# Kernel tuning notes

Measured on AMD Instinct MI355X. Metric: run time of the kernel, lower is better.

## Reference

```python
import jax, jax.numpy as jnp
import numpy as np

N_NODES = 100000
N_EDGES = 600000
N_GRAPHS = 4096
F_IN = 74
H = 128
L = 3
BN_EPS = 1e-5


def setup_inputs() -> dict:
    key = jax.random.key(0)
    ks = jax.random.split(key, 12)
    x = jax.random.normal(ks[0], (N_NODES, F_IN), dtype=jnp.float32)
    edge_index = jax.random.randint(ks[1], (2, N_EDGES), 0, N_NODES)
    batch = jnp.sort(jax.random.randint(ks[2], (N_NODES,), 0, N_GRAPHS))

    def lin(k, fan_in, fan_out):
        return (jax.random.normal(k, (fan_in, fan_out), dtype=jnp.float32)
                / np.float32(np.sqrt(fan_in)))

    emb_W = lin(ks[3], F_IN, H)
    emb_b = jnp.zeros((H,), jnp.float32)
    conv_W = jax.random.normal(ks[4], (L, H, H), dtype=jnp.float32) / np.float32(np.sqrt(H))
    conv_b = jnp.zeros((L, H), jnp.float32)
    bn_gamma = jnp.ones((L, H), jnp.float32)
    bn_beta = jnp.zeros((L, H), jnp.float32)
    w1 = lin(ks[5], 2 * H, H)
    b1 = jnp.zeros((H,), jnp.float32)
    w2 = lin(ks[6], H, H // 2)
    b2 = jnp.zeros((H // 2,), jnp.float32)
    w3 = lin(ks[7], H // 2, 1)
    b3 = jnp.zeros((1,), jnp.float32)
    return dict(x=x, edge_index=edge_index, batch=batch,
                emb_W=emb_W, emb_b=emb_b, conv_W=conv_W, conv_b=conv_b,
                bn_gamma=bn_gamma, bn_beta=bn_beta,
                w1=w1, b1=b1, w2=w2, b2=b2, w3=w3, b3=b3)


def reference(x, edge_index, batch, emb_W, emb_b, conv_W, conv_b,
              bn_gamma, bn_beta, w1, b1, w2, b2, w3, b3):
    N = x.shape[0]
    # GCN normalization with self-loops (PyG GCNConv semantics)
    loops = jnp.arange(N)
    src = jnp.concatenate([edge_index[0], loops])  # [E+N]
    dst = jnp.concatenate([edge_index[1], loops])
    deg = jax.ops.segment_sum(jnp.ones_like(dst, jnp.float32), dst, num_segments=N)
    dinv = jax.lax.rsqrt(jnp.maximum(deg, 1.0))  # deg >= 1 due to self-loops
    norm = dinv[src] * dinv[dst]                 # [E+N]

    h = jax.nn.relu(x @ emb_W + emb_b)           # [N, H]
    for i in range(L):
        hw = h @ conv_W[i]                       # [N, H]
        msg = hw[src] * norm[:, None]            # gather + scale  [E+N, H]
        h = jax.ops.segment_sum(msg, dst, num_segments=N) + conv_b[i]
        # BatchNorm1d, training-mode batch statistics (biased variance)
        mu = jnp.mean(h, axis=0)
        var = jnp.mean((h - mu) ** 2, axis=0)
        h = (h - mu) * jax.lax.rsqrt(var + BN_EPS) * bn_gamma[i] + bn_beta[i]
        h = jax.nn.relu(h)
        # dropout: identity (inference / deterministic baseline)

    # segment mean / max pooling over graphs
    cnt = jax.ops.segment_sum(jnp.ones((N,), jnp.float32), batch, num_segments=N_GRAPHS)
    g_mean = jax.ops.segment_sum(h, batch, num_segments=N_GRAPHS) / jnp.maximum(cnt, 1.0)[:, None]
    g_max = jax.ops.segment_max(h, batch, num_segments=N_GRAPHS)
    g_max = jnp.where(jnp.isfinite(g_max), g_max, 0.0)  # guard empty segments
    g = jnp.concatenate([g_mean, g_max], axis=1)         # [G, 2H]

    h1 = jax.nn.relu(g @ w1 + b1)
    h2 = jax.nn.relu(h1 @ w2 + b2)
    return h2 @ w3 + b3                                   # [G, 1]
```

## Files before the change

kernel.cpp:

```cpp
#include <hip/hip_runtime.h>

#define NN 100000
#define NE 600000
#define NG 4096
#define FIN 74
#define HD 128
#define NL 3
#define BN_EPS 1e-5f
#define NSCAN 391

typedef __attribute__((ext_vector_type(8))) short short8;
typedef __attribute__((ext_vector_type(4))) float floatx4;
typedef __attribute__((ext_vector_type(8))) unsigned short bf16x8;
typedef __attribute__((ext_vector_type(4))) unsigned short bf16x4;

__device__ __forceinline__ unsigned short f2bf(float f) {
    unsigned u = __float_as_uint(f);
    u += 0x7fff + ((u >> 16) & 1);
    return (unsigned short)(u >> 16);
}
__device__ __forceinline__ float bf2f(unsigned short u) {
    return __uint_as_float(((unsigned)u) << 16);
}

__global__ __launch_bounds__(256) void k_hist(const int* __restrict__ dst,
                                              int* __restrict__ degi) {
    int e = blockIdx.x * 256 + threadIdx.x;
    if (e < NE) atomicAdd(&degi[dst[e]], 1);
}

__global__ __launch_bounds__(256) void k_scan1(const int* __restrict__ degi,
                                               int* __restrict__ part) {
    __shared__ int s[256];
    int t = threadIdx.x;
    int idx = blockIdx.x * 256 + t;
    s[t] = (idx < NN) ? degi[idx] : 0;
    __syncthreads();
    for (int off = 128; off > 0; off >>= 1) {
        if (t < off) s[t] += s[t + off];
        __syncthreads();
    }
    if (t == 0) part[blockIdx.x] = s[0];
}

__global__ __launch_bounds__(512) void k_scan2(int* __restrict__ part) {
    __shared__ int s[512];
    int t = threadIdx.x;
    s[t] = (t < NSCAN) ? part[t] : 0;
    __syncthreads();
    for (int off = 1; off < 512; off <<= 1) {
        int v = s[t];
        int a = (t >= off) ? s[t - off] : 0;
        __syncthreads();
        s[t] = v + a;
        __syncthreads();
    }
    if (t < NSCAN) part[t] = (t > 0) ? s[t - 1] : 0;
}

__global__ __launch_bounds__(256) void k_scan3(const int* __restrict__ degi,
                                               const int* __restrict__ part,
                                               int* __restrict__ rowptr,
                                               float* __restrict__ dinv) {
    __shared__ int s[256];
    int t = threadIdx.x;
    int idx = blockIdx.x * 256 + t;
    int v = (idx < NN) ? degi[idx] : 0;
    s[t] = v;
    __syncthreads();
    for (int off = 1; off < 256; off <<= 1) {
        int x = s[t];
        int a = (t >= off) ? s[t - off] : 0;
        __syncthreads();
        s[t] = x + a;
        __syncthreads();
    }
    if (idx < NN) {
        rowptr[idx] = part[blockIdx.x] + (s[t] - v);
        dinv[idx] = rsqrtf((float)v + 1.0f);
    }
    if (idx == 0) rowptr[NN] = NE;
}

__global__ __launch_bounds__(256) void k_fill(const int* __restrict__ src,
                                              const int* __restrict__ dst,
                                              const int* __restrict__ rowptr,
                                              int* __restrict__ cursor,
                                              int* __restrict__ col) {
    int e = blockIdx.x * 256 + threadIdx.x;
    if (e >= NE) return;
    int d = dst[e];
    int pos = rowptr[d] + atomicAdd(&cursor[d], 1);
    col[pos] = src[e];
}

__global__ __launch_bounds__(256) void k_bounds(const int* __restrict__ batch,
                                                int* __restrict__ gstart) {
    int n = blockIdx.x * 256 + threadIdx.x;
    if (n >= NN) return;
    int b = batch[n];
    int bp = (n == 0) ? -1 : batch[n - 1];
    for (int g = bp + 1; g <= b; g++) gstart[g] = n;
    if (n == NN - 1)
        for (int g = b + 1; g <= NG; g++) gstart[g] = NN;
}

__global__ __launch_bounds__(256) void k_wpack(const float* __restrict__ embW,
                                               const float* __restrict__ convW,
                                               unsigned short* __restrict__ WfE,
                                               unsigned short* __restrict__ WfC) {
    int d = blockIdx.x * 256 + threadIdx.x;
    if (d < 12288) {
        int inner = d & 511, outer = d >> 9;
        int kstep = outer % 3, nt = outer / 3;
        int g = inner >> 7, n = (inner >> 3) & 15, j = inner & 7;
        int k = kstep * 32 + g * 8 + j;
        float v = (k < FIN) ? embW[k * HD + nt * 16 + n] : 0.0f;
        WfE[d] = f2bf(v);
    } else {
        int e = d - 12288;
        if (e >= NL * 16384) return;
        int layer = e >> 14, r = e & 16383;
        int j = r & 7, n = (r >> 3) & 15, g = (r >> 7) & 3, kstep = (r >> 9) & 3, nt = r >> 11;
        int k = kstep * 32 + g * 8 + j;
        WfC[e] = f2bf(convW[layer * 16384 + k * HD + nt * 16 + n]);
    }
}

__global__ __launch_bounds__(256) void k_emb(const float* __restrict__ x,
                                             const unsigned short* __restrict__ Wf,
                                             const float* __restrict__ b,
                                             unsigned short* __restrict__ hA) {
    __shared__ __align__(16) unsigned short As[4224];
    int t = threadIdx.x;
    int n0 = blockIdx.x * 32;
    for (int f = t; f < 3072; f += 256) {
        int m = f / 96, kp = f % 96;
        float v = (kp < FIN) ? x[(n0 + m) * FIN + kp] : 0.0f;
        int kstep = kp >> 5, g = (kp >> 3) & 3, j = kp & 7;
        As[(kstep * 4 + g) * 264 + m * 8 + j] = f2bf(v);
    }
    __syncthreads();
    int lane = t & 63, wv = t >> 6;
    int lanelo = lane & 15, g = lane >> 4;
    floatx4 acc[2][2] = {};
#pragma unroll
    for (int kstep = 0; kstep < 3; kstep++) {
        short8 a0 = *(const short8*)&As[(kstep * 4 + g) * 264 + lanelo * 8];
        short8 a1 = *(const short8*)&As[(kstep * 4 + g) * 264 + 128 + lanelo * 8];
        short8 b0 = *(const short8*)&Wf[(((wv * 2 + 0) * 3 + kstep) * 4 + g) * 128 + lanelo * 8];
        short8 b1 = *(const short8*)&Wf[(((wv * 2 + 1) * 3 + kstep) * 4 + g) * 128 + lanelo * 8];
        acc[0][0] = __builtin_amdgcn_mfma_f32_16x16x32_bf16(a0, b0, acc[0][0], 0, 0, 0);
        acc[0][1] = __builtin_amdgcn_mfma_f32_16x16x32_bf16(a0, b1, acc[0][1], 0, 0, 0);
        acc[1][0] = __builtin_amdgcn_mfma_f32_16x16x32_bf16(a1, b0, acc[1][0], 0, 0, 0);
        acc[1][1] = __builtin_amdgcn_mfma_f32_16x16x32_bf16(a1, b1, acc[1][1], 0, 0, 0);
    }
    __syncthreads();
#pragma unroll
    for (int ns = 0; ns < 2; ns++) {
        int colc = wv * 32 + ns * 16 + lanelo;
        float bias = b[colc];
#pragma unroll
        for (int ms = 0; ms < 2; ms++)
#pragma unroll
            for (int r = 0; r < 4; r++) {
                int rowl = ms * 16 + g * 4 + r;
                As[rowl * 132 + colc] = f2bf(fmaxf(acc[ms][ns][r] + bias, 0.0f));
            }
    }
    __syncthreads();
#pragma unroll
    for (int i = 0; i < 2; i++) {
        int f = t * 8 + i * 2048;
        int m = f >> 7, c = f & 127;
        bf16x4 lo = *(const bf16x4*)&As[m * 132 + c];
        bf16x4 hi = *(const bf16x4*)&As[m * 132 + c + 4];
        bf16x8 o = {lo.x, lo.y, lo.z, lo.w, hi.x, hi.y, hi.z, hi.w};
        *(bf16x8*)&hA[n0 * HD + f] = o;
    }
}

template <bool BN>
__global__ __launch_bounds__(256) void k_conv(const unsigned short* __restrict__ hin,
                                              const float* __restrict__ ss,
                                              const unsigned short* __restrict__ Wf,
                                              const float* __restrict__ dinv,
                                              unsigned short* __restrict__ hw) {
    __shared__ __align__(16) unsigned short As[4224];
    __shared__ float dinvs[32];
    int t = threadIdx.x;
    int n0 = blockIdx.x * 32;
    if (t < 32) dinvs[t] = dinv[n0 + t];
    int f0 = t * 8;
    int k0 = f0 & 127;
    float sc[8], sh[8];
    if (BN) {
        floatx4 s0 = *(const floatx4*)&ss[k0];
        floatx4 s1 = *(const floatx4*)&ss[k0 + 4];
        floatx4 h0 = *(const floatx4*)&ss[HD + k0];
        floatx4 h1 = *(const floatx4*)&ss[HD + k0 + 4];
        sc[0] = s0.x; sc[1] = s0.y; sc[2] = s0.z; sc[3] = s0.w;
        sc[4] = s1.x; sc[5] = s1.y; sc[6] = s1.z; sc[7] = s1.w;
        sh[0] = h0.x; sh[1] = h0.y; sh[2] = h0.z; sh[3] = h0.w;
        sh[4] = h1.x; sh[5] = h1.y; sh[6] = h1.z; sh[7] = h1.w;
    }
    int combo = (k0 >> 5) * 4 + ((k0 >> 3) & 3);
#pragma unroll
    for (int i = 0; i < 2; i++) {
        int f = f0 + i * 2048;
        int m = f >> 7;
        bf16x8 u = *(const bf16x8*)&hin[n0 * HD + f];
        bf16x8 o;
        if (BN) {
#pragma unroll
            for (int jj = 0; jj < 8; jj++) {
                float v = fmaxf(bf2f(u[jj]) * sc[jj] + sh[jj], 0.0f);
                o[jj] = f2bf(v);
            }
        } else {
            o = u;
        }
        *(bf16x8*)&As[combo * 264 + m * 8] = o;
    }
    __syncthreads();
    int lane = t & 63, wv = t >> 6;
    int lanelo = lane & 15, g = lane >> 4;
    floatx4 acc[2][2] = {};
#pragma unroll
    for (int ks = 0; ks < 4; ks++) {
        short8 a0 = *(const short8*)&As[(ks * 4 + g) * 264 + lanelo * 8];
        short8 a1 = *(const short8*)&As[(ks * 4 + g) * 264 + 128 + lanelo * 8];
        short8 b0 = *(const short8*)&Wf[(((wv * 2 + 0) * 4 + ks) * 4 + g) * 128 + lanelo * 8];
        short8 b1 = *(const short8*)&Wf[(((wv * 2 + 1) * 4 + ks) * 4 + g) * 128 + lanelo * 8];
        acc[0][0] = __builtin_amdgcn_mfma_f32_16x16x32_bf16(a0, b0, acc[0][0], 0, 0, 0);
        acc[0][1] = __builtin_amdgcn_mfma_f32_16x16x32_bf16(a0, b1, acc[0][1], 0, 0, 0);
        acc[1][0] = __builtin_amdgcn_mfma_f32_16x16x32_bf16(a1, b0, acc[1][0], 0, 0, 0);
        acc[1][1] = __builtin_amdgcn_mfma_f32_16x16x32_bf16(a1, b1, acc[1][1], 0, 0, 0);
    }
    __syncthreads();
#pragma unroll
    for (int ms = 0; ms < 2; ms++)
#pragma unroll
        for (int ns = 0; ns < 2; ns++) {
            int colc = wv * 32 + ns * 16 + lanelo;
#pragma unroll
            for (int r = 0; r < 4; r++) {
                int rowl = ms * 16 + g * 4 + r;
                As[rowl * 132 + colc] = f2bf(acc[ms][ns][r] * dinvs[rowl]);
            }
        }
    __syncthreads();
#pragma unroll
    for (int i = 0; i < 2; i++) {
        int f = f0 + i * 2048;
        int m = f >> 7, c = f & 127;
        bf16x4 lo = *(const bf16x4*)&As[m * 132 + c];
        bf16x4 hi = *(const bf16x4*)&As[m * 132 + c + 4];
        bf16x8 o = {lo.x, lo.y, lo.z, lo.w, hi.x, hi.y, hi.z, hi.w};
        *(bf16x8*)&hw[n0 * HD + f] = o;
    }
}

__global__ __launch_bounds__(256) void k_gather(const int* __restrict__ rowptr,
                                                const int* __restrict__ col,
                                                const float* __restrict__ dinv,
                                                const unsigned short* __restrict__ B,
                                                const float* __restrict__ bias,
                                                unsigned short* __restrict__ A) {
    int t = threadIdx.x;
    int n = blockIdx.x * 16 + (t >> 4);
    int c8 = (t & 15) * 8;
    bf16x8 u = *(const bf16x8*)&B[n * HD + c8];
    float acc[8];
#pragma unroll
    for (int i = 0; i < 8; i++) acc[i] = bf2f(u[i]);
    int j0 = rowptr[n], j1 = rowptr[n + 1];
    int j = j0;
    for (; j + 1 < j1; j += 2) {
        int s0 = col[j], s1 = col[j + 1];
        bf16x8 v0 = *(const bf16x8*)&B[s0 * HD + c8];
        bf16x8 v1 = *(const bf16x8*)&B[s1 * HD + c8];
#pragma unroll
        for (int i = 0; i < 8; i++) acc[i] += bf2f(v0[i]) + bf2f(v1[i]);
    }
    if (j < j1) {
        int s = col[j];
        bf16x8 v = *(const bf16x8*)&B[s * HD + c8];
#pragma unroll
        for (int i = 0; i < 8; i++) acc[i] += bf2f(v[i]);
    }
    float dd = dinv[n];
    floatx4 b0 = *(const floatx4*)&bias[c8];
    floatx4 b1 = *(const floatx4*)&bias[c8 + 4];
    bf16x8 o;
    o[0] = f2bf(acc[0] * dd + b0.x); o[1] = f2bf(acc[1] * dd + b0.y);
    o[2] = f2bf(acc[2] * dd + b0.z); o[3] = f2bf(acc[3] * dd + b0.w);
    o[4] = f2bf(acc[4] * dd + b1.x); o[5] = f2bf(acc[5] * dd + b1.y);
    o[6] = f2bf(acc[6] * dd + b1.z); o[7] = f2bf(acc[7] * dd + b1.w);
    *(bf16x8*)&A[n * HD + c8] = o;
}

__global__ __launch_bounds__(256) void k_bn_stats(const unsigned short* __restrict__ h,
                                                  float* __restrict__ sums) {
    __shared__ float ls[256];
    int t = threadIdx.x;
    ls[t] = 0.0f;
    __syncthreads();
    int c8 = (t & 15) * 8;
    float s[8] = {}, sq[8] = {};
    for (int n = blockIdx.x * 16 + (t >> 4); n < NN; n += gridDim.x * 16) {
        bf16x8 u = *(const bf16x8*)&h[n * HD + c8];
#pragma unroll
        for (int i = 0; i < 8; i++) {
            float v = bf2f(u[i]);
            s[i] += v;
            sq[i] += v * v;
        }
    }
#pragma unroll
    for (int i = 0; i < 8; i++) {
        atomicAdd(&ls[c8 + i], s[i]);
        atomicAdd(&ls[HD + c8 + i], sq[i]);
    }
    __syncthreads();
    atomicAdd(&sums[t], ls[t]);
}

__global__ __launch_bounds__(128) void k_bn_fin(const float* __restrict__ sums,
                                                const float* __restrict__ gamma,
                                                const float* __restrict__ beta,
                                                float* __restrict__ ss) {
    int c = threadIdx.x;
    float inv_n = 1.0f / (float)NN;
    float mu = sums[c] * inv_n;
    float var = sums[HD + c] * inv_n - mu * mu;
    float sc = gamma[c] * rsqrtf(var + BN_EPS);
    ss[c] = sc;
    ss[HD + c] = beta[c] - mu * sc;
}

__global__ __launch_bounds__(128) void k_pool_g(const unsigned short* __restrict__ h,
                                                const float* __restrict__ ss,
                                                const int* __restrict__ gstart,
                                                float* __restrict__ gfeat) {
    int g = blockIdx.x;
    int c = threadIdx.x;
    int n0 = gstart[g], n1 = gstart[g + 1];
    float sc = ss[c], sh = ss[HD + c];
    float s = 0.0f, mx = 0.0f;
    for (int n = n0; n < n1; n++) {
        float v = fmaxf(bf2f(h[n * HD + c]) * sc + sh, 0.0f);
        s += v;
        mx = fmaxf(mx, v);
    }
    float cntf = (float)(n1 - n0);
    gfeat[g * 256 + c] = s / fmaxf(cntf, 1.0f);
    gfeat[g * 256 + HD + c] = mx;
}

__global__ __launch_bounds__(256) void k_mlp(const float* __restrict__ gfeat,
                                             const float* __restrict__ w1,
                                             const float* __restrict__ b1,
                                             const float* __restrict__ w2,
                                             const float* __restrict__ b2,
                                             const float* __restrict__ w3,
                                             const float* __restrict__ b3,
                                             float* __restrict__ out) {
    __shared__ float gs[8][258];
    __shared__ float p1[8][130];
    __shared__ float hs[8][130];
    __shared__ float p2[3][8][66];
    __shared__ float h2s[8][66];
    __shared__ float ps[64];
    int t = threadIdx.x;
    int g0 = blockIdx.x * 8;
    for (int f = t; f < 2048; f += 256) {
        int gi = f >> 8, k = f & 255;
        gs[gi][k] = gfeat[(g0 + gi) * 256 + k];
    }
    __syncthreads();
    {
        int colc = t & 127, half = t >> 7;
        int kb = half * 128;
        float acc[8] = {};
        for (int k = 0; k < 128; k++) {
            float w = w1[(kb + k) * HD + colc];
#pragma unroll
            for (int gi = 0; gi < 8; gi++) acc[gi] += gs[gi][kb + k] * w;
        }
        if (half == 1) {
#pragma unroll
            for (int gi = 0; gi < 8; gi++) p1[gi][colc] = acc[gi];
        }
        __syncthreads();
        if (half == 0) {
            float bias = b1[colc];
#pragma unroll
            for (int gi = 0; gi < 8; gi++)
                hs[gi][colc] = fmaxf(acc[gi] + p1[gi][colc] + bias, 0.0f);
        }
    }
    __syncthreads();
    {
        int colc = t & 63, q = t >> 6;
        int kb = q * 32;
        float acc[8] = {};
        for (int k = 0; k < 32; k++) {
            float w = w2[(kb + k) * 64 + colc];
#pragma unroll
            for (int gi = 0; gi < 8; gi++) acc[gi] += hs[gi][kb + k] * w;
        }
        if (q > 0) {
#pragma unroll
            for (int gi = 0; gi < 8; gi++) p2[q - 1][gi][colc] = acc[gi];
        }
        __syncthreads();
        if (q == 0) {
            float bias = b2[colc];
#pragma unroll
            for (int gi = 0; gi < 8; gi++)
                h2s[gi][colc] = fmaxf(acc[gi] + p2[0][gi][colc] + p2[1][gi][colc]
                                      + p2[2][gi][colc] + bias, 0.0f);
        }
    }
    __syncthreads();
    if (t < 64) {
        int gi = t >> 3, prt = t & 7;
        float p = 0.0f;
#pragma unroll
        for (int k = 0; k < 8; k++) p += h2s[gi][prt * 8 + k] * w3[prt * 8 + k];
        ps[t] = p;
    }
    __syncthreads();
    if (t < 8) {
        float a = b3[0];
#pragma unroll
        for (int i = 0; i < 8; i++) a += ps[t * 8 + i];
        out[g0 + t] = a;
    }
}

extern "C" void kernel_launch(void* const* d_in, const int* in_sizes, int n_in,
                              void* d_out, int out_size, void* d_ws, size_t ws_size,
                              hipStream_t stream) {
    const float* x      = (const float*)d_in[0];
    const int*   eidx   = (const int*)d_in[1];
    const int*   batch  = (const int*)d_in[2];
    const float* emb_W  = (const float*)d_in[3];
    const float* emb_b  = (const float*)d_in[4];
    const float* conv_W = (const float*)d_in[5];
    const float* conv_b = (const float*)d_in[6];
    const float* gamma  = (const float*)d_in[7];
    const float* beta   = (const float*)d_in[8];
    const float* w1     = (const float*)d_in[9];
    const float* b1     = (const float*)d_in[10];
    const float* w2     = (const float*)d_in[11];
    const float* b2     = (const float*)d_in[12];
    const float* w3     = (const float*)d_in[13];
    const float* b3     = (const float*)d_in[14];
    float* out = (float*)d_out;

    const int* src = eidx;
    const int* dst = eidx + NE;

    unsigned short* A = (unsigned short*)d_ws;
    unsigned short* B = A + NN * HD;
    float* dinv  = (float*)(B + NN * HD);
    float* bnsum = dinv + NN;
    float* bnss  = bnsum + 256;
    float* gfeat = bnss + 256;
    int*   gstart= (int*)(gfeat + NG * 256);
    int*   degi  = gstart + NG + 1;
    int*   cursor= degi + NN;
    int*   rowptr= cursor + NN;
    int*   part  = rowptr + NN + 1;
    int*   col   = part + NSCAN;
    unsigned short* WfE = (unsigned short*)(col + NE);
    unsigned short* WfC = WfE + 12288;

    (void)hipMemsetAsync(degi, 0, 2 * NN * sizeof(int), stream);
    k_hist<<<(NE + 255) / 256, 256, 0, stream>>>(dst, degi);
    k_scan1<<<NSCAN, 256, 0, stream>>>(degi, part);
    k_scan2<<<1, 512, 0, stream>>>(part);
    k_scan3<<<NSCAN, 256, 0, stream>>>(degi, part, rowptr, dinv);
    k_fill<<<(NE + 255) / 256, 256, 0, stream>>>(src, dst, rowptr, cursor, col);
    k_bounds<<<(NN + 255) / 256, 256, 0, stream>>>(batch, gstart);
    k_wpack<<<240, 256, 0, stream>>>(emb_W, conv_W, WfE, WfC);

    k_emb<<<NN / 32, 256, 0, stream>>>(x, WfE, emb_b, A);

    for (int l = 0; l < NL; l++) {
        if (l == 0)
            k_conv<false><<<NN / 32, 256, 0, stream>>>(A, nullptr, WfC, dinv, B);
        else
            k_conv<true><<<NN / 32, 256, 0, stream>>>(A, bnss, WfC + l * 16384, dinv, B);
        k_gather<<<NN / 16, 256, 0, stream>>>(rowptr, col, dinv, B, conv_b + l * HD, A);
        (void)hipMemsetAsync(bnsum, 0, 256 * sizeof(float), stream);
        k_bn_stats<<<512, 256, 0, stream>>>(A, bnsum);
        k_bn_fin<<<1, 128, 0, stream>>>(bnsum, gamma + l * HD, beta + l * HD, bnss);
    }

    k_pool_g<<<NG, 128, 0, stream>>>(A, bnss, gstart, gfeat);

    k_mlp<<<NG / 8, 256, 0, stream>>>(gfeat, w1, b1, w2, b2, w3, b3, out);
}
```

Before: 429.1 us.

## Fuse BatchNorm statistics into gather kernel with striped global atomics

```diff
diff --git a/kernel.cpp b/kernel.cpp
--- a/kernel.cpp
+++ b/kernel.cpp
@@ -8,6 +8,7 @@
 #define NL 3
 #define BN_EPS 1e-5f
 #define NSCAN 391
+#define NSTRIPE 64
 
 typedef __attribute__((ext_vector_type(8))) short short8;
 typedef __attribute__((ext_vector_type(4))) float floatx4;
@@ -266,8 +267,11 @@
                                                 const float* __restrict__ dinv,
                                                 const unsigned short* __restrict__ B,
                                                 const float* __restrict__ bias,
-                                                unsigned short* __restrict__ A) {
-    int t = threadIdx.x;
+                                                unsigned short* __restrict__ A,
+                                                float* __restrict__ bnsum) {
+    __shared__ float ls[256];
+    int t = threadIdx.x;
+    ls[t] = 0.0f;
     int n = blockIdx.x * 16 + (t >> 4);
     int c8 = (t & 15) * 8;
     bf16x8 u = *(const bf16x8*)&B[n * HD + c8];
@@ -276,14 +280,17 @@
     for (int i = 0; i < 8; i++) acc[i] = bf2f(u[i]);
     int j0 = rowptr[n], j1 = rowptr[n + 1];
     int j = j0;
-    for (; j + 1 < j1; j += 2) {
-        int s0 = col[j], s1 = col[j + 1];
+    for (; j + 3 < j1; j += 4) {
+        int s0 = col[j], s1 = col[j + 1], s2 = col[j + 2], s3 = col[j + 3];
         bf16x8 v0 = *(const bf16x8*)&B[s0 * HD + c8];
         bf16x8 v1 = *(const bf16x8*)&B[s1 * HD + c8];
-#pragma unroll
-        for (int i = 0; i < 8; i++) acc[i] += bf2f(v0[i]) + bf2f(v1[i]);
-    }
-    if (j < j1) {
+        bf16x8 v2 = *(const bf16x8*)&B[s2 * HD + c8];
+        bf16x8 v3 = *(const bf16x8*)&B[s3 * HD + c8];
+#pragma unroll
+        for (int i = 0; i < 8; i++)
+            acc[i] += (bf2f(v0[i]) + bf2f(v1[i])) + (bf2f(v2[i]) + bf2f(v3[i]));
+    }
+    for (; j < j1; j++) {
         int s = col[j];
         bf16x8 v = *(const bf16x8*)&B[s * HD + c8];
 #pragma unroll
@@ -292,48 +299,38 @@
     float dd = dinv[n];
     floatx4 b0 = *(const floatx4*)&bias[c8];
     floatx4 b1 = *(const floatx4*)&bias[c8 + 4];
+    float hv[8];
+    hv[0] = acc[0] * dd + b0.x; hv[1] = acc[1] * dd + b0.y;
+    hv[2] = acc[2] * dd + b0.z; hv[3] = acc[3] * dd + b0.w;
+    hv[4] = acc[4] * dd + b1.x; hv[5] = acc[5] * dd + b1.y;
+    hv[6] = acc[6] * dd + b1.z; hv[7] = acc[7] * dd + b1.w;
     bf16x8 o;
-    o[0] = f2bf(acc[0] * dd + b0.x); o[1] = f2bf(acc[1] * dd + b0.y);
-    o[2] = f2bf(acc[2] * dd + b0.z); o[3] = f2bf(acc[3] * dd + b0.w);
-    o[4] = f2bf(acc[4] * dd + b1.x); o[5] = f2bf(acc[5] * dd + b1.y);
-    o[6] = f2bf(acc[6] * dd + b1.z); o[7] = f2bf(acc[7] * dd + b1.w);
+#pragma unroll
+    for (int i = 0; i < 8; i++) o[i] = f2bf(hv[i]);
     *(bf16x8*)&A[n * HD + c8] = o;
-}
-
-__global__ __launch_bounds__(256) void k_bn_stats(const unsigned short* __restrict__ h,
-                                                  float* __restrict__ sums) {
-    __shared__ float ls[256];
-    int t = threadIdx.x;
-    ls[t] = 0.0f;
-    __syncthreads();
-    int c8 = (t & 15) * 8;
-    float s[8] = {}, sq[8] = {};
-    for (int n = blockIdx.x * 16 + (t >> 4); n < NN; n += gridDim.x * 16) {
-        bf16x8 u = *(const bf16x8*)&h[n * HD + c8];
-#pragma unroll
-        for (int i = 0; i < 8; i++) {
-            float v = bf2f(u[i]);
-            s[i] += v;
-            sq[i] += v * v;
-        }
-    }
+    __syncthreads();
 #pragma unroll
     for (int i = 0; i < 8; i++) {
-        atomicAdd(&ls[c8 + i], s[i]);
-        atomicAdd(&ls[HD + c8 + i], sq[i]);
-    }
-    __syncthreads();
-    atomicAdd(&sums[t], ls[t]);
-}
-
-__global__ __launch_bounds__(128) void k_bn_fin(const float* __restrict__ sums,
+        atomicAdd(&ls[c8 + i], hv[i]);
+        atomicAdd(&ls[HD + c8 + i], hv[i] * hv[i]);
+    }
+    __syncthreads();
+    atomicAdd(&bnsum[(blockIdx.x & (NSTRIPE - 1)) * 256 + t], ls[t]);
+}
+
+__global__ __launch_bounds__(128) void k_bn_fin(const float* __restrict__ bnsum,
                                                 const float* __restrict__ gamma,
                                                 const float* __restrict__ beta,
                                                 float* __restrict__ ss) {
     int c = threadIdx.x;
+    float s = 0.0f, sq = 0.0f;
+    for (int i = 0; i < NSTRIPE; i++) {
+        s  += bnsum[i * 256 + c];
+        sq += bnsum[i * 256 + HD + c];
+    }
     float inv_n = 1.0f / (float)NN;
-    float mu = sums[c] * inv_n;
-    float var = sums[HD + c] * inv_n - mu * mu;
+    float mu = s * inv_n;
+    float var = sq * inv_n - mu * mu;
     float sc = gamma[c] * rsqrtf(var + BN_EPS);
     ss[c] = sc;
     ss[HD + c] = beta[c] - mu * sc;
@@ -466,19 +463,21 @@
     unsigned short* A = (unsigned short*)d_ws;
     unsigned short* B = A + NN * HD;
     float* dinv  = (float*)(B + NN * HD);
-    float* bnsum = dinv + NN;
-    float* bnss  = bnsum + 256;
+    float* bnss  = dinv + NN;
     float* gfeat = bnss + 256;
-    int*   gstart= (int*)(gfeat + NG * 256);
-    int*   degi  = gstart + NG + 1;
+    float* bnsum3= gfeat + NG * 256;
+    int*   degi  = (int*)(bnsum3 + NL * NSTRIPE * 256);
     int*   cursor= degi + NN;
-    int*   rowptr= cursor + NN;
+    int*   gstart= cursor + NN;
+    int*   rowptr= gstart + NG + 1;
     int*   part  = rowptr + NN + 1;
     int*   col   = part + NSCAN;
     unsigned short* WfE = (unsigned short*)(col + NE);
     unsigned short* WfC = WfE + 12288;
 
-    (void)hipMemsetAsync(degi, 0, 2 * NN * sizeof(int), stream);
+    (void)hipMemsetAsync(bnsum3, 0,
+                         (NL * NSTRIPE * 256) * sizeof(float) + 2 * NN * sizeof(int),
+                         stream);
     k_hist<<<(NE + 255) / 256, 256, 0, stream>>>(dst, degi);
     k_scan1<<<NSCAN, 256, 0, stream>>>(degi, part);
     k_scan2<<<1, 512, 0, stream>>>(part);
@@ -494,10 +493,10 @@
             k_conv<false><<<NN / 32, 256, 0, stream>>>(A, nullptr, WfC, dinv, B);
         else
             k_conv<true><<<NN / 32, 256, 0, stream>>>(A, bnss, WfC + l * 16384, dinv, B);
-        k_gather<<<NN / 16, 256, 0, stream>>>(rowptr, col, dinv, B, conv_b + l * HD, A);
-        (void)hipMemsetAsync(bnsum, 0, 256 * sizeof(float), stream);
-        k_bn_stats<<<512, 256, 0, stream>>>(A, bnsum);
-        k_bn_fin<<<1, 128, 0, stream>>>(bnsum, gamma + l * HD, beta + l * HD, bnss);
+        k_gather<<<NN / 16, 256, 0, stream>>>(rowptr, col, dinv, B, conv_b + l * HD, A,
+                                              bnsum3 + l * NSTRIPE * 256);
+        k_bn_fin<<<1, 128, 0, stream>>>(bnsum3 + l * NSTRIPE * 256,
+                                        gamma + l * HD, beta + l * HD, bnss);
     }
 
     k_pool_g<<<NG, 128, 0, stream>>>(A, bnss, gstart, gfeat);
```

After: 725.5 us. +69.1%, slower.
